# Kernel optimization log

Measured on AMD Instinct MI355X. Metric: run time of the kernel, lower is better.

## Reference

```python
import jax, jax.numpy as jnp
import numpy as np

IN_DIM, H, OUT_DIM = 64, 128, 64
B, T = 1024, 512
NEG_SLOPE = 0.01
LN_EPS = 1e-5


def _mlp_layer(x, W, b, g, beta):
    h = x @ W.T + b
    h = jnp.where(h > 0, h, NEG_SLOPE * h)  # LeakyReLU
    mu = h.mean(-1, keepdims=True)
    var = h.var(-1, keepdims=True)
    return g * (h - mu) / jnp.sqrt(var + LN_EPS) + beta


def setup_inputs() -> dict:
    key = jax.random.key(0)
    ks = jax.random.split(key, 16)
    s = 1.0 / np.sqrt(H)
    return {
        "x": jax.random.normal(ks[0], (B, T, IN_DIM), jnp.float32),
        "is_init": jax.random.randint(ks[1], (B, T, 1), 0, 2) > 0,
        "hx": jax.random.normal(ks[2], (B, H), jnp.float32),
        "W1": jax.random.uniform(ks[3], (H, IN_DIM), jnp.float32, -s, s),
        "b1": jnp.zeros((H,), jnp.float32),
        "g1": jnp.ones((H,), jnp.float32),
        "beta1": jnp.zeros((H,), jnp.float32),
        "W2": jax.random.uniform(ks[4], (H, H), jnp.float32, -s, s),
        "b2": jnp.zeros((H,), jnp.float32),
        "g2": jnp.ones((H,), jnp.float32),
        "beta2": jnp.zeros((H,), jnp.float32),
        "W_ih": jax.random.uniform(ks[5], (3 * H, H), jnp.float32, -s, s),
        "W_hh": jax.random.uniform(ks[6], (3 * H, H), jnp.float32, -s, s),
        "b_ih": jax.random.uniform(ks[7], (3 * H,), jnp.float32, -s, s),
        "b_hh": jax.random.uniform(ks[8], (3 * H,), jnp.float32, -s, s),
        "W_out": jax.random.uniform(ks[9], (OUT_DIM, H), jnp.float32, -s, s),
        "b_out": jnp.zeros((OUT_DIM,), jnp.float32),
    }


def reference(x, is_init, hx, W1, b1, g1, beta1, W2, b2, g2, beta2,
              W_ih, W_hh, b_ih, b_hh, W_out, b_out):
    # MLP: two (Linear -> LeakyReLU -> LayerNorm) layers, width 128
    h = _mlp_layer(x, W1, b1, g1, beta1)
    h = _mlp_layer(h, W2, b2, g2, beta2)

    # Precompute input-side gate preactivations for all timesteps: [B,T,3H]
    gates_x = h @ W_ih.T + b_ih
    gates_x_t = jnp.swapaxes(gates_x, 0, 1)      # [T,B,3H]
    init_t = jnp.swapaxes(is_init, 0, 1)         # [T,B,1]

    def step(h_prev, inp):
        gx, init = inp
        h_prev = jnp.where(init, 0.0, h_prev)    # reset-on-init
        gh = h_prev @ W_hh.T + b_hh
        xr, xz, xn = jnp.split(gx, 3, axis=-1)
        hr, hz, hn = jnp.split(gh, 3, axis=-1)
        r = jax.nn.sigmoid(xr + hr)
        z = jax.nn.sigmoid(xz + hz)
        n = jnp.tanh(xn + r * hn)
        h_new = (1.0 - z) * n + z * h_prev
        return h_new, h_new

    hx_final, ys = jax.lax.scan(step, hx, (gates_x_t, init_t))
    y = jnp.swapaxes(ys, 0, 1)                   # [B,T,H]
    out = y @ W_out.T + b_out                    # [B,T,OUT_DIM]
    return out, hx_final
```

## Files before the change

### kernel.cpp

```cpp
#include <hip/hip_runtime.h>
#include <hip/hip_bf16.h>

#define IN_DIM 64
#define H 128
#define G3 384
#define OUT_DIM 64
#define Bb 1024
#define Tt 512
#define NEG 0.01f
#define EPSLN 1e-5f

#define CHUNK 16
#define NCHUNK (Tt / CHUNK)
#define BPB 2

typedef __bf16 bf16_t;
typedef __bf16 bf16x8 __attribute__((ext_vector_type(8)));
typedef float f32x4 __attribute__((ext_vector_type(4)));

#define GXS 392
#define GX_OFF 0
#define HAS 136
#define HA_OFF 25088
#define HPB_OFF 33792
#define RED_OFF 42496
#define MNR_OFF 43520
#define VEC_OFF 43776
#define INI_OFF 50176
#define SMEM_BYTES 50320

#define V_B1 0
#define V_G1 128
#define V_BE1 256
#define V_B2 384
#define V_G2 512
#define V_BE2 640
#define V_BIH 768
#define V_BHH 1152
#define V_BOUT 1536

#define WS_W1 0
#define WS_W2 8192
#define WS_WIH 24576
#define WS_WHH 73728
#define WS_WOUT 122880
#define WS_ELEMS 131072

#define MFMA(a, b, c) __builtin_amdgcn_mfma_f32_16x16x32_bf16((a), (b), (c), 0, 0, 0)

template <bool WSB>
__device__ __forceinline__ bf16x8 ldfrag(const float* pf, const bf16_t* pb) {
    if constexpr (WSB) {
        return *(const bf16x8*)pb;
    } else {
        bf16x8 f;
#pragma unroll
        for (int j = 0; j < 8; ++j) f[j] = (bf16_t)pf[j];
        return f;
    }
}

__global__ void cvt_weights(const float* __restrict__ W1, const float* __restrict__ W2,
                            const float* __restrict__ Wih, const float* __restrict__ Whh,
                            const float* __restrict__ Wout, bf16_t* __restrict__ ws) {
    int i = blockIdx.x * 256 + threadIdx.x;
    float v;
    if (i < WS_W2) v = W1[i];
    else if (i < WS_WIH) v = W2[i - WS_W2];
    else if (i < WS_WHH) v = Wih[i - WS_WIH];
    else if (i < WS_WOUT) v = Whh[i - WS_WHH];
    else v = Wout[i - WS_WOUT];
    ws[i] = (bf16_t)v;
}

template <bool WSB>
__global__ void __launch_bounds__(256, 2) gru_fused(
    const float* __restrict__ x, const int* __restrict__ is_init,
    const float* __restrict__ hx,
    const float* __restrict__ W1, const float* __restrict__ b1,
    const float* __restrict__ g1, const float* __restrict__ be1,
    const float* __restrict__ W2, const float* __restrict__ b2,
    const float* __restrict__ g2, const float* __restrict__ be2,
    const float* __restrict__ Wih, const float* __restrict__ Whh,
    const float* __restrict__ bih, const float* __restrict__ bhh,
    const float* __restrict__ Wout, const float* __restrict__ bout,
    const bf16_t* __restrict__ wsb,
    float* __restrict__ out)
{
    extern __shared__ char smem[];
    bf16_t* GX  = (bf16_t*)(smem + GX_OFF);
    bf16_t* HA  = (bf16_t*)(smem + HA_OFF);
    bf16_t* HPB = (bf16_t*)(smem + HPB_OFF);
    float*  RED = (float*) (smem + RED_OFF);
    float*  MNR = (float*) (smem + MNR_OFF);
    float*  VEC = (float*) (smem + VEC_OFF);
    int*    INI = (int*)   (smem + INI_OFF);

    const bf16_t* W1B  = wsb + WS_W1;
    const bf16_t* W2B  = wsb + WS_W2;
    const bf16_t* WihB = wsb + WS_WIH;
    const bf16_t* WhhB = wsb + WS_WHH;
    const bf16_t* WoB  = wsb + WS_WOUT;

    const int tid  = threadIdx.x;
    const int w    = tid >> 6;
    const int lane = tid & 63;
    const int ln   = lane & 15;
    const int quad = lane >> 4;
    const int b0   = blockIdx.x * BPB;

    for (int i = tid; i < H; i += 256) {
        VEC[V_B1 + i] = b1[i];  VEC[V_G1 + i] = g1[i];  VEC[V_BE1 + i] = be1[i];
        VEC[V_B2 + i] = b2[i];  VEC[V_G2 + i] = g2[i];  VEC[V_BE2 + i] = be2[i];
    }
    for (int i = tid; i < G3; i += 256) {
        VEC[V_BIH + i] = bih[i];  VEC[V_BHH + i] = bhh[i];
    }
    if (tid < OUT_DIM) VEC[V_BOUT + tid] = bout[tid];
    for (int i = tid; i < 2 * 16 * HAS; i += 256) HPB[i] = (bf16_t)0.f;
    __syncthreads();

    float hp[2] = {0.f, 0.f};
    if (quad < BPB) {
        int b = quad;
        int im = is_init[(size_t)(b0 + b) * Tt];
#pragma unroll
        for (int sub = 0; sub < 2; ++sub) {
            int j = w * 32 + sub * 16 + ln;
            float v = im ? 0.f : hx[(size_t)(b0 + b) * H + j];
            hp[sub] = v;
            HPB[b * 4 * HAS + j] = (bf16_t)v;
        }
    }
    float bh[3][2];
#pragma unroll
    for (int g = 0; g < 3; ++g)
#pragma unroll
        for (int sub = 0; sub < 2; ++sub)
            bh[g][sub] = bhh[g * H + w * 32 + sub * 16 + ln];

    bf16x8 whhf[6][4];
#pragma unroll
    for (int ntl = 0; ntl < 6; ++ntl) {
        int gate = ntl >> 1, sub = ntl & 1;
        int n = gate * H + w * 32 + sub * 16 + ln;
#pragma unroll
        for (int ks = 0; ks < 4; ++ks) {
            size_t off = (size_t)n * H + ks * 32 + quad * 8;
            whhf[ntl][ks] = ldfrag<WSB>(Whh + off, WhhB + off);
        }
    }
    __syncthreads();

    for (int tc = 0; tc < NCHUNK; ++tc) {
        const int t0 = tc * CHUNK;

        f32x4 vs[BPB][2];

        {
            bf16x8 w1f[2][2];
#pragma unroll
            for (int ntl = 0; ntl < 2; ++ntl) {
                int n = w * 32 + ntl * 16 + ln;
#pragma unroll
                for (int ks = 0; ks < 2; ++ks) {
                    size_t off = (size_t)n * IN_DIM + ks * 32 + quad * 8;
                    w1f[ntl][ks] = ldfrag<WSB>(W1 + off, W1B + off);
                }
            }
#pragma unroll
            for (int mt = 0; mt < BPB; ++mt) {
                const float* xr_ = x + ((size_t)(b0 + mt) * Tt + t0 + ln) * IN_DIM;
                bf16x8 a0, a1;
#pragma unroll
                for (int j = 0; j < 8; ++j) {
                    a0[j] = (bf16_t)xr_[quad * 8 + j];
                    a1[j] = (bf16_t)xr_[32 + quad * 8 + j];
                }
#pragma unroll
                for (int ntl = 0; ntl < 2; ++ntl) {
                    f32x4 c = {0.f, 0.f, 0.f, 0.f};
                    c = MFMA(a0, w1f[ntl][0], c);
                    c = MFMA(a1, w1f[ntl][1], c);
                    vs[mt][ntl] = c;
                }
            }
            float bv[2], gv[2], bev[2];
#pragma unroll
            for (int ntl = 0; ntl < 2; ++ntl) {
                int n = w * 32 + ntl * 16 + ln;
                bv[ntl] = VEC[V_B1 + n]; gv[ntl] = VEC[V_G1 + n]; bev[ntl] = VEC[V_BE1 + n];
            }
#pragma unroll
            for (int mt = 0; mt < BPB; ++mt) {
#pragma unroll
                for (int reg = 0; reg < 4; ++reg) {
                    float v0 = vs[mt][0][reg] + bv[0]; v0 = v0 > 0.f ? v0 : NEG * v0;
                    float v1 = vs[mt][1][reg] + bv[1]; v1 = v1 > 0.f ? v1 : NEG * v1;
                    vs[mt][0][reg] = v0; vs[mt][1][reg] = v1;
                    float s = v0 + v1, q = v0 * v0 + v1 * v1;
#pragma unroll
                    for (int d = 1; d < 16; d <<= 1) { s += __shfl_xor(s, d); q += __shfl_xor(q, d); }
                    if (ln == 0) {
                        int rr = mt * 16 + quad * 4 + reg;
                        RED[rr * 8 + w] = s; RED[rr * 8 + 4 + w] = q;
                    }
                }
            }
            __syncthreads();
            if (tid < 32) {
                float s = RED[tid * 8] + RED[tid * 8 + 1] + RED[tid * 8 + 2] + RED[tid * 8 + 3];
                float q = RED[tid * 8 + 4] + RED[tid * 8 + 5] + RED[tid * 8 + 6] + RED[tid * 8 + 7];
                float mean = s * (1.f / H);
                float var = q * (1.f / H) - mean * mean;
                MNR[tid * 2] = mean; MNR[tid * 2 + 1] = rsqrtf(var + EPSLN);
            }
            __syncthreads();
#pragma unroll
            for (int mt = 0; mt < BPB; ++mt) {
#pragma unroll
                for (int reg = 0; reg < 4; ++reg) {
                    int rr = mt * 16 + quad * 4 + reg;
                    float mean = MNR[rr * 2], rstd = MNR[rr * 2 + 1];
#pragma unroll
                    for (int ntl = 0; ntl < 2; ++ntl) {
                        int n = w * 32 + ntl * 16 + ln;
                        HA[rr * HAS + n] = (bf16_t)(gv[ntl] * (vs[mt][ntl][reg] - mean) * rstd + bev[ntl]);
                    }
                }
            }
            __syncthreads();
        }

        {
            bf16x8 w2f[2][4];
#pragma unroll
            for (int ntl = 0; ntl < 2; ++ntl) {
                int n = w * 32 + ntl * 16 + ln;
#pragma unroll
                for (int ks = 0; ks < 4; ++ks) {
                    size_t off = (size_t)n * H + ks * 32 + quad * 8;
                    w2f[ntl][ks] = ldfrag<WSB>(W2 + off, W2B + off);
                }
            }
#pragma unroll
            for (int mt = 0; mt < BPB; ++mt) {
                bf16x8 af[4];
#pragma unroll
                for (int ks = 0; ks < 4; ++ks)
                    af[ks] = *(const bf16x8*)(HA + (mt * 16 + ln) * HAS + ks * 32 + quad * 8);
#pragma unroll
                for (int ntl = 0; ntl < 2; ++ntl) {
                    f32x4 c = {0.f, 0.f, 0.f, 0.f};
#pragma unroll
                    for (int ks = 0; ks < 4; ++ks) c = MFMA(af[ks], w2f[ntl][ks], c);
                    vs[mt][ntl] = c;
                }
            }
            float bv[2], gv[2], bev[2];
#pragma unroll
            for (int ntl = 0; ntl < 2; ++ntl) {
                int n = w * 32 + ntl * 16 + ln;
                bv[ntl] = VEC[V_B2 + n]; gv[ntl] = VEC[V_G2 + n]; bev[ntl] = VEC[V_BE2 + n];
            }
#pragma unroll
            for (int mt = 0; mt < BPB; ++mt) {
#pragma unroll
                for (int reg = 0; reg < 4; ++reg) {
                    float v0 = vs[mt][0][reg] + bv[0]; v0 = v0 > 0.f ? v0 : NEG * v0;
                    float v1 = vs[mt][1][reg] + bv[1]; v1 = v1 > 0.f ? v1 : NEG * v1;
                    vs[mt][0][reg] = v0; vs[mt][1][reg] = v1;
                    float s = v0 + v1, q = v0 * v0 + v1 * v1;
#pragma unroll
                    for (int d = 1; d < 16; d <<= 1) { s += __shfl_xor(s, d); q += __shfl_xor(q, d); }
                    if (ln == 0) {
                        int rr = mt * 16 + quad * 4 + reg;
                        RED[rr * 8 + w] = s; RED[rr * 8 + 4 + w] = q;
                    }
                }
            }
            __syncthreads();
            if (tid < 32) {
                float s = RED[tid * 8] + RED[tid * 8 + 1] + RED[tid * 8 + 2] + RED[tid * 8 + 3];
                float q = RED[tid * 8 + 4] + RED[tid * 8 + 5] + RED[tid * 8 + 6] + RED[tid * 8 + 7];
                float mean = s * (1.f / H);
                float var = q * (1.f / H) - mean * mean;
                MNR[tid * 2] = mean; MNR[tid * 2 + 1] = rsqrtf(var + EPSLN);
            }
            __syncthreads();
#pragma unroll
            for (int mt = 0; mt < BPB; ++mt) {
#pragma unroll
                for (int reg = 0; reg < 4; ++reg) {
                    int rr = mt * 16 + quad * 4 + reg;
                    float mean = MNR[rr * 2], rstd = MNR[rr * 2 + 1];
#pragma unroll
                    for (int ntl = 0; ntl < 2; ++ntl) {
                        int n = w * 32 + ntl * 16 + ln;
                        HA[rr * HAS + n] = (bf16_t)(gv[ntl] * (vs[mt][ntl][reg] - mean) * rstd + bev[ntl]);
                    }
                }
            }
            __syncthreads();
        }

#pragma unroll
        for (int half = 0; half < 2; ++half) {
            bf16x8 wf[3][4];
            float bv[3];
#pragma unroll
            for (int k3 = 0; k3 < 3; ++k3) {
                int n = (w * 6 + half * 3 + k3) * 16 + ln;
                bv[k3] = VEC[V_BIH + n];
#pragma unroll
                for (int ks = 0; ks < 4; ++ks) {
                    size_t off = (size_t)n * H + ks * 32 + quad * 8;
                    wf[k3][ks] = ldfrag<WSB>(Wih + off, WihB + off);
                }
            }
#pragma unroll
            for (int mt = 0; mt < BPB; ++mt) {
                bf16x8 af[4];
#pragma unroll
                for (int ks = 0; ks < 4; ++ks)
                    af[ks] = *(const bf16x8*)(HA + (mt * 16 + ln) * HAS + ks * 32 + quad * 8);
#pragma unroll
                for (int k3 = 0; k3 < 3; ++k3) {
                    int n = (w * 6 + half * 3 + k3) * 16 + ln;
                    f32x4 c = {0.f, 0.f, 0.f, 0.f};
#pragma unroll
                    for (int ks = 0; ks < 4; ++ks) c = MFMA(af[ks], wf[k3][ks], c);
#pragma unroll
                    for (int reg = 0; reg < 4; ++reg)
                        GX[(mt * 16 + quad * 4 + reg) * GXS + n] = (bf16_t)(c[reg] + bv[k3]);
                }
            }
        }
        if (tid < BPB * 17) {
            int b = tid / 17, s = tid % 17;
            int t = t0 + s;
            INI[tid] = (t < Tt) ? is_init[(size_t)(b0 + b) * Tt + t] : 0;
        }

        for (int s = 0; s < CHUNK; ++s) {
            __syncthreads();
            const int t = t0 + s;
            const int rp = t & 1;
            bf16x8 af[4];
#pragma unroll
            for (int ks = 0; ks < 4; ++ks)
                af[ks] = *(const bf16x8*)(HPB + rp * 16 * HAS + ln * HAS + ks * 32 + quad * 8);
            f32x4 gc[6];
#pragma unroll
            for (int ntl = 0; ntl < 6; ++ntl) {
                f32x4 c = {0.f, 0.f, 0.f, 0.f};
#pragma unroll
                for (int ks = 0; ks < 4; ++ks) c = MFMA(af[ks], whhf[ntl][ks], c);
                gc[ntl] = c;
            }
            if (quad < BPB) {
                const int b = quad;
                bf16_t* hw = HPB + (rp ^ 1) * 16 * HAS + b * 4 * HAS;
                const int rbase = (b * 16 + s) * GXS;
#pragma unroll
                for (int sub = 0; sub < 2; ++sub) {
                    int j = w * 32 + sub * 16 + ln;
                    float xr = (float)GX[rbase + j];
                    float xz = (float)GX[rbase + H + j];
                    float xn = (float)GX[rbase + 2 * H + j];
                    float hr = gc[sub][0]     + bh[0][sub];
                    float hz = gc[2 + sub][0] + bh[1][sub];
                    float hn = gc[4 + sub][0] + bh[2][sub];
                    float r = 1.f / (1.f + __expf(-(xr + hr)));
                    float z = 1.f / (1.f + __expf(-(xz + hz)));
                    float a = xn + r * hn;
                    a = fminf(fmaxf(a, -15.f), 15.f);
                    float e = __expf(-2.f * a);
                    float nn = (1.f - e) / (1.f + e);
                    float hnew = (1.f - z) * nn + z * hp[sub];
                    HA[(b * 16 + s) * HAS + j] = (bf16_t)hnew;
                    float hm;
                    if (t < Tt - 1) {
                        hm = INI[b * 17 + s + 1] ? 0.f : hnew;
                    } else {
                        hm = hnew;
                        out[(size_t)Bb * Tt * OUT_DIM + (size_t)(b0 + b) * H + j] = hnew;
                    }
                    hp[sub] = hm;
                    hw[j] = (bf16_t)hm;
                }
            }
        }
        __syncthreads();

        {
            int o = w * 16 + ln;
            size_t ob = (size_t)o * H;
            bf16x8 wof[4];
#pragma unroll
            for (int ks = 0; ks < 4; ++ks)
                wof[ks] = ldfrag<WSB>(Wout + ob + ks * 32 + quad * 8, WoB + ob + ks * 32 + quad * 8);
            float bo = VEC[V_BOUT + o];
#pragma unroll
            for (int mt = 0; mt < BPB; ++mt) {
                bf16x8 af[4];
#pragma unroll
                for (int ks = 0; ks < 4; ++ks)
                    af[ks] = *(const bf16x8*)(HA + (mt * 16 + ln) * HAS + ks * 32 + quad * 8);
                f32x4 c = {0.f, 0.f, 0.f, 0.f};
#pragma unroll
                for (int ks = 0; ks < 4; ++ks) c = MFMA(af[ks], wof[ks], c);
#pragma unroll
                for (int reg = 0; reg < 4; ++reg)
                    out[((size_t)(b0 + mt) * Tt + t0 + quad * 4 + reg) * OUT_DIM + o] = c[reg] + bo;
            }
        }
        __syncthreads();
    }
}

extern "C" void kernel_launch(void* const* d_in, const int* in_sizes, int n_in,
                              void* d_out, int out_size, void* d_ws, size_t ws_size,
                              hipStream_t stream) {
    const float* x      = (const float*)d_in[0];
    const int*   is_init= (const int*)  d_in[1];
    const float* hx     = (const float*)d_in[2];
    const float* W1     = (const float*)d_in[3];
    const float* b1     = (const float*)d_in[4];
    const float* g1     = (const float*)d_in[5];
    const float* be1    = (const float*)d_in[6];
    const float* W2     = (const float*)d_in[7];
    const float* b2     = (const float*)d_in[8];
    const float* g2     = (const float*)d_in[9];
    const float* be2    = (const float*)d_in[10];
    const float* Wih    = (const float*)d_in[11];
    const float* Whh    = (const float*)d_in[12];
    const float* bih    = (const float*)d_in[13];
    const float* bhh    = (const float*)d_in[14];
    const float* Wout   = (const float*)d_in[15];
    const float* bout   = (const float*)d_in[16];
    float* out = (float*)d_out;

    const bool usews = (d_ws != nullptr) && (ws_size >= (size_t)(WS_ELEMS * sizeof(bf16_t)));
    if (usews) {
        bf16_t* ws = (bf16_t*)d_ws;
        cvt_weights<<<WS_ELEMS / 256, 256, 0, stream>>>(W1, W2, Wih, Whh, Wout, ws);
        hipFuncSetAttribute((const void*)gru_fused<true>,
                            hipFuncAttributeMaxDynamicSharedMemorySize, SMEM_BYTES);
        gru_fused<true><<<Bb / BPB, 256, SMEM_BYTES, stream>>>(
            x, is_init, hx, W1, b1, g1, be1, W2, b2, g2, be2,
            Wih, Whh, bih, bhh, Wout, bout, ws, out);
    } else {
        hipFuncSetAttribute((const void*)gru_fused<false>,
                            hipFuncAttributeMaxDynamicSharedMemorySize, SMEM_BYTES);
        gru_fused<false><<<Bb / BPB, 256, SMEM_BYTES, stream>>>(
            x, is_init, hx, W1, b1, g1, be1, W2, b2, g2, be2,
            Wih, Whh, bih, bhh, Wout, bout, nullptr, out);
    }
}
```

Baseline: 1.402 ms.

## Parallelize GRU scan over time tiles with speculative pass and fix-up passes

Replaces the sequential per-batch scan with a time-tiled scheme. All 32 time tiles run in parallel from a zero (or reset) initial state, and each tile records its end state and whether it starts with a reset. A fix-up kernel reruns the prefix of each tile up to the first reset, using the previous tile's end state, and a sweep kernel propagates corrections for tiles whose state depends on earlier tiles. This exposes far more parallelism than one block per two batch rows. In exchange it adds redundant MLP and GRU recomputation, extra workspace traffic and a sequential sweep whose cost depends on how often resets occur.

```diff
diff --git a/kernel.cpp b/kernel.cpp
--- a/kernel.cpp
+++ b/kernel.cpp
@@ -11,33 +11,13 @@
 #define EPSLN 1e-5f
 
 #define CHUNK 16
-#define NCHUNK (Tt / CHUNK)
-#define BPB 2
+#define NTILE (Tt / CHUNK)
 
 typedef __bf16 bf16_t;
 typedef __bf16 bf16x8 __attribute__((ext_vector_type(8)));
 typedef float f32x4 __attribute__((ext_vector_type(4)));
 
-#define GXS 392
-#define GX_OFF 0
-#define HAS 136
-#define HA_OFF 25088
-#define HPB_OFF 33792
-#define RED_OFF 42496
-#define MNR_OFF 43520
-#define VEC_OFF 43776
-#define INI_OFF 50176
-#define SMEM_BYTES 50320
-
-#define V_B1 0
-#define V_G1 128
-#define V_BE1 256
-#define V_B2 384
-#define V_G2 512
-#define V_BE2 640
-#define V_BIH 768
-#define V_BHH 1152
-#define V_BOUT 1536
+#define MFMA(a, b, c) __builtin_amdgcn_mfma_f32_16x16x32_bf16((a), (b), (c), 0, 0, 0)
 
 #define WS_W1 0
 #define WS_W2 8192
@@ -45,24 +25,18 @@
 #define WS_WHH 73728
 #define WS_WOUT 122880
 #define WS_ELEMS 131072
-
-#define MFMA(a, b, c) __builtin_amdgcn_mfma_f32_16x16x32_bf16((a), (b), (c), 0, 0, 0)
-
-template <bool WSB>
-__device__ __forceinline__ bf16x8 ldfrag(const float* pf, const bf16_t* pb) {
-    if constexpr (WSB) {
-        return *(const bf16x8*)pb;
-    } else {
-        bf16x8 f;
-#pragma unroll
-        for (int j = 0; j < 8; ++j) f[j] = (bf16_t)pf[j];
-        return f;
-    }
-}
+#define WS_E_OFF 262144
+#define WS_R_OFF (WS_E_OFF + 16777216)
+#define WS_RA_OFF (WS_R_OFF + 131072)
+#define WS_NEED (WS_RA_OFF + 131072)
+
+#define HAS 136
+#define GXS 392
 
 __global__ void cvt_weights(const float* __restrict__ W1, const float* __restrict__ W2,
                             const float* __restrict__ Wih, const float* __restrict__ Whh,
-                            const float* __restrict__ Wout, bf16_t* __restrict__ ws) {
+                            const float* __restrict__ Wout, bf16_t* __restrict__ ws,
+                            int* __restrict__ RA) {
     int i = blockIdx.x * 256 + threadIdx.x;
     float v;
     if (i < WS_W2) v = W1[i];
@@ -71,10 +45,764 @@
     else if (i < WS_WOUT) v = Whh[i - WS_WHH];
     else v = Wout[i - WS_WOUT];
     ws[i] = (bf16_t)v;
+    if (i < Bb * NTILE) RA[i] = 0;
 }
 
-template <bool WSB>
-__global__ void __launch_bounds__(256, 2) gru_fused(
+#define P1_GX 0
+#define P1_HA 50176
+#define P1_HPB 67584
+#define P1_RED 76288
+#define P1_MNR 78336
+#define P1_INI 78848
+#define P1_SMEM 79120
+#define BPB1 4
+
+__global__ void __launch_bounds__(256, 2) gru_pass1(
+    const float* __restrict__ x, const int* __restrict__ is_init,
+    const float* __restrict__ hx,
+    const float* __restrict__ b1, const float* __restrict__ g1, const float* __restrict__ be1,
+    const float* __restrict__ b2, const float* __restrict__ g2, const float* __restrict__ be2,
+    const float* __restrict__ bih, const float* __restrict__ bhh,
+    const float* __restrict__ bout,
+    const bf16_t* __restrict__ wsb,
+    float* __restrict__ E, int* __restrict__ R,
+    float* __restrict__ out)
+{
+    extern __shared__ char smem[];
+    bf16_t* GX  = (bf16_t*)(smem + P1_GX);
+    bf16_t* HA  = (bf16_t*)(smem + P1_HA);
+    bf16_t* HPB = (bf16_t*)(smem + P1_HPB);
+    float*  RED = (float*) (smem + P1_RED);
+    float*  MNR = (float*) (smem + P1_MNR);
+    int*    INI = (int*)   (smem + P1_INI);
+
+    const bf16_t* W1B  = wsb + WS_W1;
+    const bf16_t* W2B  = wsb + WS_W2;
+    const bf16_t* WihB = wsb + WS_WIH;
+    const bf16_t* WhhB = wsb + WS_WHH;
+    const bf16_t* WoB  = wsb + WS_WOUT;
+
+    const int tid  = threadIdx.x;
+    const int w    = tid >> 6;
+    const int lane = tid & 63;
+    const int ln   = lane & 15;
+    const int quad = lane >> 4;
+    const int b0   = blockIdx.x * BPB1;
+    const int tile = blockIdx.y;
+    const int t0   = tile * CHUNK;
+
+    for (int i = tid; i < 2 * 16 * HAS; i += 256) HPB[i] = (bf16_t)0.f;
+    __syncthreads();
+
+    float hp[2] = {0.f, 0.f};
+    if (tile == 0) {
+        const int b = quad;
+        int im = is_init[(size_t)(b0 + b) * Tt];
+#pragma unroll
+        for (int sub = 0; sub < 2; ++sub) {
+            int j = w * 32 + sub * 16 + ln;
+            float v = im ? 0.f : hx[(size_t)(b0 + b) * H + j];
+            hp[sub] = v;
+            HPB[b * 4 * HAS + j] = (bf16_t)v;
+        }
+    }
+    float bh[3][2];
+#pragma unroll
+    for (int g = 0; g < 3; ++g)
+#pragma unroll
+        for (int sub = 0; sub < 2; ++sub)
+            bh[g][sub] = bhh[g * H + w * 32 + sub * 16 + ln];
+
+    bf16x8 whhf[6][4];
+#pragma unroll
+    for (int ntl = 0; ntl < 6; ++ntl) {
+        int gate = ntl >> 1, sub = ntl & 1;
+        int n = gate * H + w * 32 + sub * 16 + ln;
+#pragma unroll
+        for (int ks = 0; ks < 4; ++ks)
+            whhf[ntl][ks] = *(const bf16x8*)(WhhB + (size_t)n * H + ks * 32 + quad * 8);
+    }
+    __syncthreads();
+
+    f32x4 vs[BPB1][2];
+
+    {
+        bf16x8 w1f[2][2];
+#pragma unroll
+        for (int ntl = 0; ntl < 2; ++ntl) {
+            int n = w * 32 + ntl * 16 + ln;
+#pragma unroll
+            for (int ks = 0; ks < 2; ++ks)
+                w1f[ntl][ks] = *(const bf16x8*)(W1B + (size_t)n * IN_DIM + ks * 32 + quad * 8);
+        }
+#pragma unroll
+        for (int mt = 0; mt < BPB1; ++mt) {
+            const float* xr_ = x + ((size_t)(b0 + mt) * Tt + t0 + ln) * IN_DIM;
+            bf16x8 a0, a1;
+#pragma unroll
+            for (int j = 0; j < 8; ++j) {
+                a0[j] = (bf16_t)xr_[quad * 8 + j];
+                a1[j] = (bf16_t)xr_[32 + quad * 8 + j];
+            }
+#pragma unroll
+            for (int ntl = 0; ntl < 2; ++ntl) {
+                f32x4 c = {0.f, 0.f, 0.f, 0.f};
+                c = MFMA(a0, w1f[ntl][0], c);
+                c = MFMA(a1, w1f[ntl][1], c);
+                vs[mt][ntl] = c;
+            }
+        }
+        float bv[2], gv[2], bev[2];
+#pragma unroll
+        for (int ntl = 0; ntl < 2; ++ntl) {
+            int n = w * 32 + ntl * 16 + ln;
+            bv[ntl] = b1[n]; gv[ntl] = g1[n]; bev[ntl] = be1[n];
+        }
+#pragma unroll
+        for (int mt = 0; mt < BPB1; ++mt) {
+#pragma unroll
+            for (int reg = 0; reg < 4; ++reg) {
+                float v0 = vs[mt][0][reg] + bv[0]; v0 = v0 > 0.f ? v0 : NEG * v0;
+                float v1 = vs[mt][1][reg] + bv[1]; v1 = v1 > 0.f ? v1 : NEG * v1;
+                vs[mt][0][reg] = v0; vs[mt][1][reg] = v1;
+                float s = v0 + v1, q = v0 * v0 + v1 * v1;
+#pragma unroll
+                for (int d = 1; d < 16; d <<= 1) { s += __shfl_xor(s, d); q += __shfl_xor(q, d); }
+                if (ln == 0) {
+                    int rr = mt * 16 + quad * 4 + reg;
+                    RED[rr * 8 + w] = s; RED[rr * 8 + 4 + w] = q;
+                }
+            }
+        }
+        __syncthreads();
+        if (tid < 64) {
+            float s = RED[tid * 8] + RED[tid * 8 + 1] + RED[tid * 8 + 2] + RED[tid * 8 + 3];
+            float q = RED[tid * 8 + 4] + RED[tid * 8 + 5] + RED[tid * 8 + 6] + RED[tid * 8 + 7];
+            float mean = s * (1.f / H);
+            float var = q * (1.f / H) - mean * mean;
+            MNR[tid * 2] = mean; MNR[tid * 2 + 1] = rsqrtf(var + EPSLN);
+        }
+        __syncthreads();
+#pragma unroll
+        for (int mt = 0; mt < BPB1; ++mt) {
+#pragma unroll
+            for (int reg = 0; reg < 4; ++reg) {
+                int rr = mt * 16 + quad * 4 + reg;
+                float mean = MNR[rr * 2], rstd = MNR[rr * 2 + 1];
+#pragma unroll
+                for (int ntl = 0; ntl < 2; ++ntl) {
+                    int n = w * 32 + ntl * 16 + ln;
+                    HA[rr * HAS + n] = (bf16_t)(gv[ntl] * (vs[mt][ntl][reg] - mean) * rstd + bev[ntl]);
+                }
+            }
+        }
+        __syncthreads();
+    }
+
+    {
+        bf16x8 w2f[2][4];
+#pragma unroll
+        for (int ntl = 0; ntl < 2; ++ntl) {
+            int n = w * 32 + ntl * 16 + ln;
+#pragma unroll
+            for (int ks = 0; ks < 4; ++ks)
+                w2f[ntl][ks] = *(const bf16x8*)(W2B + (size_t)n * H + ks * 32 + quad * 8);
+        }
+#pragma unroll
+        for (int mt = 0; mt < BPB1; ++mt) {
+            bf16x8 af[4];
+#pragma unroll
+            for (int ks = 0; ks < 4; ++ks)
+                af[ks] = *(const bf16x8*)(HA + (mt * 16 + ln) * HAS + ks * 32 + quad * 8);
+#pragma unroll
+            for (int ntl = 0; ntl < 2; ++ntl) {
+                f32x4 c = {0.f, 0.f, 0.f, 0.f};
+#pragma unroll
+                for (int ks = 0; ks < 4; ++ks) c = MFMA(af[ks], w2f[ntl][ks], c);
+                vs[mt][ntl] = c;
+            }
+        }
+        float bv[2], gv[2], bev[2];
+#pragma unroll
+        for (int ntl = 0; ntl < 2; ++ntl) {
+            int n = w * 32 + ntl * 16 + ln;
+            bv[ntl] = b2[n]; gv[ntl] = g2[n]; bev[ntl] = be2[n];
+        }
+#pragma unroll
+        for (int mt = 0; mt < BPB1; ++mt) {
+#pragma unroll
+            for (int reg = 0; reg < 4; ++reg) {
+                float v0 = vs[mt][0][reg] + bv[0]; v0 = v0 > 0.f ? v0 : NEG * v0;
+                float v1 = vs[mt][1][reg] + bv[1]; v1 = v1 > 0.f ? v1 : NEG * v1;
+                vs[mt][0][reg] = v0; vs[mt][1][reg] = v1;
+                float s = v0 + v1, q = v0 * v0 + v1 * v1;
+#pragma unroll
+                for (int d = 1; d < 16; d <<= 1) { s += __shfl_xor(s, d); q += __shfl_xor(q, d); }
+                if (ln == 0) {
+                    int rr = mt * 16 + quad * 4 + reg;
+                    RED[rr * 8 + w] = s; RED[rr * 8 + 4 + w] = q;
+                }
+            }
+        }
+        __syncthreads();
+        if (tid < 64) {
+            float s = RED[tid * 8] + RED[tid * 8 + 1] + RED[tid * 8 + 2] + RED[tid * 8 + 3];
+            float q = RED[tid * 8 + 4] + RED[tid * 8 + 5] + RED[tid * 8 + 6] + RED[tid * 8 + 7];
+            float mean = s * (1.f / H);
+            float var = q * (1.f / H) - mean * mean;
+            MNR[tid * 2] = mean; MNR[tid * 2 + 1] = rsqrtf(var + EPSLN);
+        }
+        __syncthreads();
+#pragma unroll
+        for (int mt = 0; mt < BPB1; ++mt) {
+#pragma unroll
+            for (int reg = 0; reg < 4; ++reg) {
+                int rr = mt * 16 + quad * 4 + reg;
+                float mean = MNR[rr * 2], rstd = MNR[rr * 2 + 1];
+#pragma unroll
+                for (int ntl = 0; ntl < 2; ++ntl) {
+                    int n = w * 32 + ntl * 16 + ln;
+                    HA[rr * HAS + n] = (bf16_t)(gv[ntl] * (vs[mt][ntl][reg] - mean) * rstd + bev[ntl]);
+                }
+            }
+        }
+        __syncthreads();
+    }
+
+#pragma unroll
+    for (int half = 0; half < 2; ++half) {
+        bf16x8 wf[3][4];
+        float bv[3];
+#pragma unroll
+        for (int k3 = 0; k3 < 3; ++k3) {
+            int n = (w * 6 + half * 3 + k3) * 16 + ln;
+            bv[k3] = bih[n];
+#pragma unroll
+            for (int ks = 0; ks < 4; ++ks)
+                wf[k3][ks] = *(const bf16x8*)(WihB + (size_t)n * H + ks * 32 + quad * 8);
+        }
+#pragma unroll
+        for (int mt = 0; mt < BPB1; ++mt) {
+            bf16x8 af[4];
+#pragma unroll
+            for (int ks = 0; ks < 4; ++ks)
+                af[ks] = *(const bf16x8*)(HA + (mt * 16 + ln) * HAS + ks * 32 + quad * 8);
+#pragma unroll
+            for (int k3 = 0; k3 < 3; ++k3) {
+                int n = (w * 6 + half * 3 + k3) * 16 + ln;
+                f32x4 c = {0.f, 0.f, 0.f, 0.f};
+#pragma unroll
+                for (int ks = 0; ks < 4; ++ks) c = MFMA(af[ks], wf[k3][ks], c);
+#pragma unroll
+                for (int reg = 0; reg < 4; ++reg)
+                    GX[(mt * 16 + quad * 4 + reg) * GXS + n] = (bf16_t)(c[reg] + bv[k3]);
+            }
+        }
+    }
+    if (tid < BPB1 * 17) {
+        int b = tid / 17, s = tid % 17;
+        int t = t0 + s;
+        INI[tid] = (t < Tt) ? is_init[(size_t)(b0 + b) * Tt + t] : 0;
+    }
+
+    for (int s = 0; s < CHUNK; ++s) {
+        __syncthreads();
+        const int t = t0 + s;
+        const int rp = t & 1;
+        bf16x8 af[4];
+#pragma unroll
+        for (int ks = 0; ks < 4; ++ks)
+            af[ks] = *(const bf16x8*)(HPB + rp * 16 * HAS + ln * HAS + ks * 32 + quad * 8);
+        f32x4 gc[6];
+#pragma unroll
+        for (int ntl = 0; ntl < 6; ++ntl) {
+            f32x4 c = {0.f, 0.f, 0.f, 0.f};
+#pragma unroll
+            for (int ks = 0; ks < 4; ++ks) c = MFMA(af[ks], whhf[ntl][ks], c);
+            gc[ntl] = c;
+        }
+        {
+            const int b = quad;
+            bf16_t* hw = HPB + (rp ^ 1) * 16 * HAS + b * 4 * HAS;
+            const int rbase = (b * 16 + s) * GXS;
+#pragma unroll
+            for (int sub = 0; sub < 2; ++sub) {
+                int j = w * 32 + sub * 16 + ln;
+                float xr = (float)GX[rbase + j];
+                float xz = (float)GX[rbase + H + j];
+                float xn = (float)GX[rbase + 2 * H + j];
+                float hr = gc[sub][0]     + bh[0][sub];
+                float hz = gc[2 + sub][0] + bh[1][sub];
+                float hn = gc[4 + sub][0] + bh[2][sub];
+                float r = 1.f / (1.f + __expf(-(xr + hr)));
+                float z = 1.f / (1.f + __expf(-(xz + hz)));
+                float a = xn + r * hn;
+                a = fminf(fmaxf(a, -15.f), 15.f);
+                float e = __expf(-2.f * a);
+                float nn = (1.f - e) / (1.f + e);
+                float hnew = (1.f - z) * nn + z * hp[sub];
+                HA[(b * 16 + s) * HAS + j] = (bf16_t)hnew;
+                float hm;
+                if (s < CHUNK - 1) {
+                    hm = INI[b * 17 + s + 1] ? 0.f : hnew;
+                } else {
+                    hm = hnew;
+                    E[((size_t)(b0 + b) * NTILE + tile) * H + j] = hnew;
+                }
+                hp[sub] = hm;
+                hw[j] = (bf16_t)hm;
+            }
+        }
+    }
+    __syncthreads();
+
+    if (tid < BPB1) {
+        int any = 0;
+#pragma unroll
+        for (int s = 0; s < CHUNK; ++s) any |= INI[tid * 17 + s];
+        R[(b0 + tid) * NTILE + tile] = (tile == 0) ? 1 : (any ? 1 : 0);
+    }
+
+    {
+        int o = w * 16 + ln;
+        bf16x8 wof[4];
+#pragma unroll
+        for (int ks = 0; ks < 4; ++ks)
+            wof[ks] = *(const bf16x8*)(WoB + (size_t)o * H + ks * 32 + quad * 8);
+        float bo = bout[o];
+#pragma unroll
+        for (int mt = 0; mt < BPB1; ++mt) {
+            bf16x8 af[4];
+#pragma unroll
+            for (int ks = 0; ks < 4; ++ks)
+                af[ks] = *(const bf16x8*)(HA + (mt * 16 + ln) * HAS + ks * 32 + quad * 8);
+            f32x4 c = {0.f, 0.f, 0.f, 0.f};
+#pragma unroll
+            for (int ks = 0; ks < 4; ++ks) c = MFMA(af[ks], wof[ks], c);
+#pragma unroll
+            for (int reg = 0; reg < 4; ++reg)
+                out[((size_t)(b0 + mt) * Tt + t0 + quad * 4 + reg) * OUT_DIM + o] = c[reg] + bo;
+        }
+    }
+}
+
+__global__ void __launch_bounds__(256, 2) gru_fixp(
+    const float* __restrict__ x, const int* __restrict__ is_init,
+    const float* __restrict__ b1, const float* __restrict__ g1, const float* __restrict__ be1,
+    const float* __restrict__ b2, const float* __restrict__ g2, const float* __restrict__ be2,
+    const float* __restrict__ bih, const float* __restrict__ bhh,
+    const float* __restrict__ bout,
+    const bf16_t* __restrict__ wsb,
+    float* __restrict__ E, const int* __restrict__ R, int* __restrict__ RA,
+    float* __restrict__ out)
+{
+    __shared__ bf16_t sHA[16 * HAS];
+    __shared__ bf16_t sHPB[2][16 * HAS];
+    __shared__ float  sHPF[16 * 128];
+    __shared__ float  sRED[16 * 8];
+    __shared__ float  sMNR[16 * 2];
+    __shared__ int    sINI[16 * 16];
+    __shared__ int    sF[16];
+    __shared__ int    sNeed[16];
+    __shared__ int    sAny, sMaxf;
+
+    const bf16_t* W1B  = wsb + WS_W1;
+    const bf16_t* W2B  = wsb + WS_W2;
+    const bf16_t* WihB = wsb + WS_WIH;
+    const bf16_t* WhhB = wsb + WS_WHH;
+    const bf16_t* WoB  = wsb + WS_WOUT;
+
+    const int tid  = threadIdx.x;
+    const int w    = tid >> 6;
+    const int lane = tid & 63;
+    const int ln   = lane & 15;
+    const int quad = lane >> 4;
+    const int bB   = blockIdx.x * 16;
+    const int i    = blockIdx.y + 1;
+    const int t0   = i * CHUNK;
+
+    {
+        int b = tid >> 4, s = tid & 15;
+        sINI[tid] = is_init[(size_t)(bB + b) * Tt + t0 + s];
+    }
+    if (tid < 16) sNeed[tid] = R[(bB + tid) * NTILE + (i - 1)];
+    if (tid == 0) { sAny = 0; sMaxf = 0; }
+    __syncthreads();
+    if (tid < 16) {
+        int f = 16;
+        for (int s = 15; s >= 0; --s) if (sINI[tid * 16 + s]) f = s;
+        sF[tid] = f;
+        int need = (sNeed[tid] && f > 0) ? 1 : 0;
+        sNeed[tid] = need;
+        if (need) { atomicOr(&sAny, 1); atomicMax(&sMaxf, f); }
+    }
+    __syncthreads();
+    if (!sAny) return;
+    const int maxf = sMaxf;
+
+    for (int idx = tid; idx < 16 * 128; idx += 256) {
+        int b = idx >> 7, j = idx & 127;
+        float v = sNeed[b] ? E[((size_t)(bB + b) * NTILE + i - 1) * H + j] : 0.f;
+        sHPF[idx] = v;
+        sHPB[0][b * HAS + j] = (bf16_t)v;
+        sHPB[1][b * HAS + j] = (bf16_t)0.f;
+    }
+
+    float bh[3][2], bihv[6];
+#pragma unroll
+    for (int g = 0; g < 3; ++g)
+#pragma unroll
+        for (int sub = 0; sub < 2; ++sub) {
+            int j = w * 32 + sub * 16 + ln;
+            bh[g][sub] = bhh[g * H + j];
+            bihv[g * 2 + sub] = bih[g * H + j];
+        }
+    float bv1[2], gv1[2], bev1[2], bv2[2], gv2[2], bev2[2];
+#pragma unroll
+    for (int ntl = 0; ntl < 2; ++ntl) {
+        int n = w * 32 + ntl * 16 + ln;
+        bv1[ntl] = b1[n]; gv1[ntl] = g1[n]; bev1[ntl] = be1[n];
+        bv2[ntl] = b2[n]; gv2[ntl] = g2[n]; bev2[ntl] = be2[n];
+    }
+    bf16x8 whhf[6][4];
+#pragma unroll
+    for (int ntl = 0; ntl < 6; ++ntl) {
+        int gate = ntl >> 1, sub = ntl & 1;
+        int n = gate * H + w * 32 + sub * 16 + ln;
+#pragma unroll
+        for (int ks = 0; ks < 4; ++ks)
+            whhf[ntl][ks] = *(const bf16x8*)(WhhB + (size_t)n * H + ks * 32 + quad * 8);
+    }
+    bf16x8 wof[4];
+    {
+        int o = w * 16 + ln;
+#pragma unroll
+        for (int ks = 0; ks < 4; ++ks)
+            wof[ks] = *(const bf16x8*)(WoB + (size_t)o * H + ks * 32 + quad * 8);
+    }
+    float bo = bout[w * 16 + ln];
+    __syncthreads();
+
+    for (int s = 0; s < maxf; ++s) {
+        const int t = t0 + s;
+        const int par = s & 1;
+        f32x4 vs[2];
+
+        {
+            const float* xr_ = x + ((size_t)(bB + ln) * Tt + t) * IN_DIM;
+            bf16x8 a0, a1;
+#pragma unroll
+            for (int j = 0; j < 8; ++j) {
+                a0[j] = (bf16_t)xr_[quad * 8 + j];
+                a1[j] = (bf16_t)xr_[32 + quad * 8 + j];
+            }
+#pragma unroll
+            for (int ntl = 0; ntl < 2; ++ntl) {
+                int n = w * 32 + ntl * 16 + ln;
+                bf16x8 f0 = *(const bf16x8*)(W1B + (size_t)n * IN_DIM + quad * 8);
+                bf16x8 f1 = *(const bf16x8*)(W1B + (size_t)n * IN_DIM + 32 + quad * 8);
+                f32x4 c = {0.f, 0.f, 0.f, 0.f};
+                c = MFMA(a0, f0, c);
+                c = MFMA(a1, f1, c);
+                vs[ntl] = c;
+            }
+        }
+#pragma unroll
+        for (int reg = 0; reg < 4; ++reg) {
+            float v0 = vs[0][reg] + bv1[0]; v0 = v0 > 0.f ? v0 : NEG * v0;
+            float v1 = vs[1][reg] + bv1[1]; v1 = v1 > 0.f ? v1 : NEG * v1;
+            vs[0][reg] = v0; vs[1][reg] = v1;
+            float sm = v0 + v1, q = v0 * v0 + v1 * v1;
+#pragma unroll
+            for (int d = 1; d < 16; d <<= 1) { sm += __shfl_xor(sm, d); q += __shfl_xor(q, d); }
+            if (ln == 0) {
+                int rr = quad * 4 + reg;
+                sRED[rr * 8 + w] = sm; sRED[rr * 8 + 4 + w] = q;
+            }
+        }
+        __syncthreads();
+        if (tid < 16) {
+            float sm = sRED[tid * 8] + sRED[tid * 8 + 1] + sRED[tid * 8 + 2] + sRED[tid * 8 + 3];
+            float q = sRED[tid * 8 + 4] + sRED[tid * 8 + 5] + sRED[tid * 8 + 6] + sRED[tid * 8 + 7];
+            float mean = sm * (1.f / H);
+            float var = q * (1.f / H) - mean * mean;
+            sMNR[tid * 2] = mean; sMNR[tid * 2 + 1] = rsqrtf(var + EPSLN);
+        }
+        __syncthreads();
+#pragma unroll
+        for (int reg = 0; reg < 4; ++reg) {
+            int rr = quad * 4 + reg;
+            float mean = sMNR[rr * 2], rstd = sMNR[rr * 2 + 1];
+#pragma unroll
+            for (int ntl = 0; ntl < 2; ++ntl) {
+                int n = w * 32 + ntl * 16 + ln;
+                sHA[rr * HAS + n] = (bf16_t)(gv1[ntl] * (vs[ntl][reg] - mean) * rstd + bev1[ntl]);
+            }
+        }
+        __syncthreads();
+
+        {
+            bf16x8 af[4];
+#pragma unroll
+            for (int ks = 0; ks < 4; ++ks)
+                af[ks] = *(const bf16x8*)(sHA + ln * HAS + ks * 32 + quad * 8);
+#pragma unroll
+            for (int ntl = 0; ntl < 2; ++ntl) {
+                int n = w * 32 + ntl * 16 + ln;
+                f32x4 c = {0.f, 0.f, 0.f, 0.f};
+#pragma unroll
+                for (int ks = 0; ks < 4; ++ks) {
+                    bf16x8 f = *(const bf16x8*)(W2B + (size_t)n * H + ks * 32 + quad * 8);
+                    c = MFMA(af[ks], f, c);
+                }
+                vs[ntl] = c;
+            }
+        }
+        __syncthreads();
+#pragma unroll
+        for (int reg = 0; reg < 4; ++reg) {
+            float v0 = vs[0][reg] + bv2[0]; v0 = v0 > 0.f ? v0 : NEG * v0;
+            float v1 = vs[1][reg] + bv2[1]; v1 = v1 > 0.f ? v1 : NEG * v1;
+            vs[0][reg] = v0; vs[1][reg] = v1;
+            float sm = v0 + v1, q = v0 * v0 + v1 * v1;
+#pragma unroll
+            for (int d = 1; d < 16; d <<= 1) { sm += __shfl_xor(sm, d); q += __shfl_xor(q, d); }
+            if (ln == 0) {
+                int rr = quad * 4 + reg;
+                sRED[rr * 8 + w] = sm; sRED[rr * 8 + 4 + w] = q;
+            }
+        }
+        __syncthreads();
+        if (tid < 16) {
+            float sm = sRED[tid * 8] + sRED[tid * 8 + 1] + sRED[tid * 8 + 2] + sRED[tid * 8 + 3];
+            float q = sRED[tid * 8 + 4] + sRED[tid * 8 + 5] + sRED[tid * 8 + 6] + sRED[tid * 8 + 7];
+            float mean = sm * (1.f / H);
+            float var = q * (1.f / H) - mean * mean;
+            sMNR[tid * 2] = mean; sMNR[tid * 2 + 1] = rsqrtf(var + EPSLN);
+        }
+        __syncthreads();
+#pragma unroll
+        for (int reg = 0; reg < 4; ++reg) {
+            int rr = quad * 4 + reg;
+            float mean = sMNR[rr * 2], rstd = sMNR[rr * 2 + 1];
+#pragma unroll
+            for (int ntl = 0; ntl < 2; ++ntl) {
+                int n = w * 32 + ntl * 16 + ln;
+                sHA[rr * HAS + n] = (bf16_t)(gv2[ntl] * (vs[ntl][reg] - mean) * rstd + bev2[ntl]);
+            }
+        }
+        __syncthreads();
+
+        bf16x8 af2[4], afh[4];
+#pragma unroll
+        for (int ks = 0; ks < 4; ++ks) {
+            af2[ks] = *(const bf16x8*)(sHA + ln * HAS + ks * 32 + quad * 8);
+            afh[ks] = *(const bf16x8*)(sHPB[par] + ln * HAS + ks * 32 + quad * 8);
+        }
+        f32x4 gxc[6], ghc[6];
+#pragma unroll
+        for (int ntl = 0; ntl < 6; ++ntl) {
+            int gate = ntl >> 1, sub = ntl & 1;
+            int n = gate * H + w * 32 + sub * 16 + ln;
+            f32x4 cg = {0.f, 0.f, 0.f, 0.f};
+#pragma unroll
+            for (int ks = 0; ks < 4; ++ks) {
+                bf16x8 f = *(const bf16x8*)(WihB + (size_t)n * H + ks * 32 + quad * 8);
+                cg = MFMA(af2[ks], f, cg);
+            }
+            gxc[ntl] = cg;
+            f32x4 ch = {0.f, 0.f, 0.f, 0.f};
+#pragma unroll
+            for (int ks = 0; ks < 4; ++ks) ch = MFMA(afh[ks], whhf[ntl][ks], ch);
+            ghc[ntl] = ch;
+        }
+        __syncthreads();
+
+#pragma unroll
+        for (int reg = 0; reg < 4; ++reg) {
+            const int b = quad * 4 + reg;
+            const int msk = sNeed[b] && (s < sF[b]);
+#pragma unroll
+            for (int sub = 0; sub < 2; ++sub) {
+                int j = w * 32 + sub * 16 + ln;
+                float xr = gxc[sub][reg]     + bihv[sub];
+                float xz = gxc[2 + sub][reg] + bihv[2 + sub];
+                float xn = gxc[4 + sub][reg] + bihv[4 + sub];
+                float hr = ghc[sub][reg]     + bh[0][sub];
+                float hz = ghc[2 + sub][reg] + bh[1][sub];
+                float hn = ghc[4 + sub][reg] + bh[2][sub];
+                float r = 1.f / (1.f + __expf(-(xr + hr)));
+                float z = 1.f / (1.f + __expf(-(xz + hz)));
+                float a = xn + r * hn;
+                a = fminf(fmaxf(a, -15.f), 15.f);
+                float e = __expf(-2.f * a);
+                float nn = (1.f - e) / (1.f + e);
+                float hp = sHPF[b * 128 + j];
+                float hnew = (1.f - z) * nn + z * hp;
+                if (msk) {
+                    sHPF[b * 128 + j] = hnew;
+                    sHPB[par ^ 1][b * HAS + j] = (bf16_t)hnew;
+                    sHA[b * HAS + j] = (bf16_t)hnew;
+                }
+            }
+        }
+        __syncthreads();
+
+        {
+            bf16x8 af[4];
+#pragma unroll
+            for (int ks = 0; ks < 4; ++ks)
+                af[ks] = *(const bf16x8*)(sHA + ln * HAS + ks * 32 + quad * 8);
+            f32x4 c = {0.f, 0.f, 0.f, 0.f};
+#pragma unroll
+            for (int ks = 0; ks < 4; ++ks) c = MFMA(af[ks], wof[ks], c);
+            int o = w * 16 + ln;
+#pragma unroll
+            for (int reg = 0; reg < 4; ++reg) {
+                int b = quad * 4 + reg;
+                if (sNeed[b] && s < sF[b])
+                    out[((size_t)(bB + b) * Tt + t) * OUT_DIM + o] = c[reg] + bo;
+            }
+        }
+        __syncthreads();
+    }
+
+    for (int idx = tid; idx < 16 * 128; idx += 256) {
+        int b = idx >> 7, j = idx & 127;
+        if (sNeed[b] && sF[b] == 16)
+            E[((size_t)(bB + b) * NTILE + i) * H + j] = sHPF[b * 128 + j];
+    }
+    if (tid < 16 && sNeed[tid] && sF[tid] == 16)
+        RA[(bB + tid) * NTILE + i] = 1;
+}
+
+__global__ void __launch_bounds__(128) gru_sweep(
+    const float* __restrict__ x, const int* __restrict__ is_init,
+    const float* __restrict__ W1, const float* __restrict__ b1,
+    const float* __restrict__ g1, const float* __restrict__ be1,
+    const float* __restrict__ W2, const float* __restrict__ b2,
+    const float* __restrict__ g2, const float* __restrict__ be2,
+    const float* __restrict__ Wih, const float* __restrict__ Whh,
+    const float* __restrict__ bih, const float* __restrict__ bhh,
+    const float* __restrict__ Wout, const float* __restrict__ bout,
+    const float* __restrict__ E, const int* __restrict__ R, const int* __restrict__ RA,
+    float* __restrict__ out)
+{
+    __shared__ float sX[64], sH1[128], sH2[128], sHH[128], sRS[4];
+    __shared__ int sI[16], sFf;
+
+    const int b = blockIdx.x;
+    const int j = threadIdx.x;
+    const int wv = j >> 6, lj = j & 63;
+
+    float h = E[((size_t)b * NTILE) * H + j];
+
+    for (int i = 1; i < NTILE; ++i) {
+        int Rm1 = R[b * NTILE + i - 1];
+        if (!Rm1) {
+            if (j < 16) sI[j] = is_init[(size_t)b * Tt + i * CHUNK + j];
+            __syncthreads();
+            if (j == 0) {
+                int f = 16;
+                for (int s = 15; s >= 0; --s) if (sI[s]) f = s;
+                sFf = f;
+            }
+            __syncthreads();
+            int f = sFf;
+            for (int s = 0; s < f; ++s) {
+                int t = i * CHUNK + s;
+                sHH[j] = h;
+                if (j < 64) sX[j] = x[((size_t)b * Tt + t) * IN_DIM + j];
+                __syncthreads();
+                float a1 = b1[j];
+                const float* w1r = W1 + (size_t)j * IN_DIM;
+                for (int k = 0; k < 64; ++k) a1 += sX[k] * w1r[k];
+                a1 = a1 > 0.f ? a1 : NEG * a1;
+                {
+                    float sv = a1, sq = a1 * a1;
+                    for (int d = 1; d < 64; d <<= 1) { sv += __shfl_xor(sv, d); sq += __shfl_xor(sq, d); }
+                    if (lj == 0) { sRS[wv * 2] = sv; sRS[wv * 2 + 1] = sq; }
+                    __syncthreads();
+                    float mean = (sRS[0] + sRS[2]) * (1.f / H);
+                    float var = (sRS[1] + sRS[3]) * (1.f / H) - mean * mean;
+                    a1 = g1[j] * (a1 - mean) * rsqrtf(var + EPSLN) + be1[j];
+                }
+                sH1[j] = a1;
+                __syncthreads();
+                float a2 = b2[j];
+                const float* w2r = W2 + (size_t)j * H;
+                for (int k = 0; k < 128; ++k) a2 += sH1[k] * w2r[k];
+                a2 = a2 > 0.f ? a2 : NEG * a2;
+                {
+                    float sv = a2, sq = a2 * a2;
+                    for (int d = 1; d < 64; d <<= 1) { sv += __shfl_xor(sv, d); sq += __shfl_xor(sq, d); }
+                    if (lj == 0) { sRS[wv * 2] = sv; sRS[wv * 2 + 1] = sq; }
+                    __syncthreads();
+                    float mean = (sRS[0] + sRS[2]) * (1.f / H);
+                    float var = (sRS[1] + sRS[3]) * (1.f / H) - mean * mean;
+                    a2 = g2[j] * (a2 - mean) * rsqrtf(var + EPSLN) + be2[j];
+                }
+                sH2[j] = a2;
+                __syncthreads();
+                float gx0 = bih[j], gx1 = bih[H + j], gx2 = bih[2 * H + j];
+                float gh0 = bhh[j], gh1 = bhh[H + j], gh2 = bhh[2 * H + j];
+                const float* wi0 = Wih + (size_t)j * H;
+                const float* wi1 = Wih + (size_t)(H + j) * H;
+                const float* wi2 = Wih + (size_t)(2 * H + j) * H;
+                const float* wh0 = Whh + (size_t)j * H;
+                const float* wh1 = Whh + (size_t)(H + j) * H;
+                const float* wh2 = Whh + (size_t)(2 * H + j) * H;
+                for (int k = 0; k < 128; ++k) {
+                    float h2k = sH2[k], hhk = sHH[k];
+                    gx0 += h2k * wi0[k]; gx1 += h2k * wi1[k]; gx2 += h2k * wi2[k];
+                    gh0 += hhk * wh0[k]; gh1 += hhk * wh1[k]; gh2 += hhk * wh2[k];
+                }
+                float r = 1.f / (1.f + __expf(-(gx0 + gh0)));
+                float z = 1.f / (1.f + __expf(-(gx1 + gh1)));
+                float a = gx2 + r * gh2;
+                a = fminf(fmaxf(a, -15.f), 15.f);
+                float e = __expf(-2.f * a);
+                float nn = (1.f - e) / (1.f + e);
+                h = (1.f - z) * nn + z * h;
+                __syncthreads();
+                sH1[j] = h;
+                __syncthreads();
+                if (j < 64) {
+                    float o = bout[j];
+                    const float* wo = Wout + (size_t)j * H;
+                    for (int k = 0; k < 128; ++k) o += sH1[k] * wo[k];
+                    out[((size_t)b * Tt + t) * OUT_DIM + j] = o;
+                }
+                __syncthreads();
+            }
+            if (f < 16) h = E[((size_t)b * NTILE + i) * H + j];
+        } else {
+            if (R[b * NTILE + i] || RA[b * NTILE + i])
+                h = E[((size_t)b * NTILE + i) * H + j];
+        }
+    }
+    out[(size_t)Bb * Tt * OUT_DIM + (size_t)b * H + j] = h;
+}
+
+#define FGX_OFF 0
+#define FHA_OFF 25088
+#define FHPB_OFF 33792
+#define FRED_OFF 42496
+#define FMNR_OFF 43520
+#define FVEC_OFF 43776
+#define FINI_OFF 50176
+#define FSMEM 50320
+#define FV_B1 0
+#define FV_G1 128
+#define FV_BE1 256
+#define FV_B2 384
+#define FV_G2 512
+#define FV_BE2 640
+#define FV_BIH 768
+#define FV_BHH 1152
+#define FV_BOUT 1536
+
+__global__ void __launch_bounds__(256, 2) gru_seq(
     const float* __restrict__ x, const int* __restrict__ is_init,
     const float* __restrict__ hx,
     const float* __restrict__ W1, const float* __restrict__ b1,
@@ -84,52 +812,45 @@
     const float* __restrict__ Wih, const float* __restrict__ Whh,
     const float* __restrict__ bih, const float* __restrict__ bhh,
     const float* __restrict__ Wout, const float* __restrict__ bout,
-    const bf16_t* __restrict__ wsb,
     float* __restrict__ out)
 {
     extern __shared__ char smem[];
-    bf16_t* GX  = (bf16_t*)(smem + GX_OFF);
-    bf16_t* HA  = (bf16_t*)(smem + HA_OFF);
-    bf16_t* HPB = (bf16_t*)(smem + HPB_OFF);
-    float*  RED = (float*) (smem + RED_OFF);
-    float*  MNR = (float*) (smem + MNR_OFF);
-    float*  VEC = (float*) (smem + VEC_OFF);
-    int*    INI = (int*)   (smem + INI_OFF);
-
-    const bf16_t* W1B  = wsb + WS_W1;
-    const bf16_t* W2B  = wsb + WS_W2;
-    const bf16_t* WihB = wsb + WS_WIH;
-    const bf16_t* WhhB = wsb + WS_WHH;
-    const bf16_t* WoB  = wsb + WS_WOUT;
+    bf16_t* GX  = (bf16_t*)(smem + FGX_OFF);
+    bf16_t* HA  = (bf16_t*)(smem + FHA_OFF);
+    bf16_t* HPB = (bf16_t*)(smem + FHPB_OFF);
+    float*  RED = (float*) (smem + FRED_OFF);
+    float*  MNR = (float*) (smem + FMNR_OFF);
+    float*  VEC = (float*) (smem + FVEC_OFF);
+    int*    INI = (int*)   (smem + FINI_OFF);
 
     const int tid  = threadIdx.x;
     const int w    = tid >> 6;
     const int lane = tid & 63;
     const int ln   = lane & 15;
     const int quad = lane >> 4;
-    const int b0   = blockIdx.x * BPB;
+    const int b0   = blockIdx.x * 2;
 
     for (int i = tid; i < H; i += 256) {
-        VEC[V_B1 + i] = b1[i];  VEC[V_G1 + i] = g1[i];  VEC[V_BE1 + i] = be1[i];
-        VEC[V_B2 + i] = b2[i];  VEC[V_G2 + i] = g2[i];  VEC[V_BE2 + i] = be2[i];
+        VEC[FV_B1 + i] = b1[i];  VEC[FV_G1 + i] = g1[i];  VEC[FV_BE1 + i] = be1[i];
+        VEC[FV_B2 + i] = b2[i];  VEC[FV_G2 + i] = g2[i];  VEC[FV_BE2 + i] = be2[i];
     }
     for (int i = tid; i < G3; i += 256) {
-        VEC[V_BIH + i] = bih[i];  VEC[V_BHH + i] = bhh[i];
-    }
-    if (tid < OUT_DIM) VEC[V_BOUT + tid] = bout[tid];
+        VEC[FV_BIH + i] = bih[i];  VEC[FV_BHH + i] = bhh[i];
+    }
+    if (tid < OUT_DIM) VEC[FV_BOUT + tid] = bout[tid];
     for (int i = tid; i < 2 * 16 * HAS; i += 256) HPB[i] = (bf16_t)0.f;
     __syncthreads();
 
     float hp[2] = {0.f, 0.f};
-    if (quad < BPB) {
+    if (quad < 2) {
         int b = quad;
         int im = is_init[(size_t)(b0 + b) * Tt];
 #pragma unroll
         for (int sub = 0; sub < 2; ++sub) {
-            int j = w * 32 + sub * 16 + ln;
-            float v = im ? 0.f : hx[(size_t)(b0 + b) * H + j];
+            int jj = w * 32 + sub * 16 + ln;
+            float v = im ? 0.f : hx[(size_t)(b0 + b) * H + jj];
             hp[sub] = v;
-            HPB[b * 4 * HAS + j] = (bf16_t)v;
+            HPB[b * 4 * HAS + jj] = (bf16_t)v;
         }
     }
     float bh[3][2];
@@ -144,38 +865,44 @@
     for (int ntl = 0; ntl < 6; ++ntl) {
         int gate = ntl >> 1, sub = ntl & 1;
         int n = gate * H + w * 32 + sub * 16 + ln;
+        const float* p = Whh + (size_t)n * H;
 #pragma unroll
         for (int ks = 0; ks < 4; ++ks) {
-            size_t off = (size_t)n * H + ks * 32 + quad * 8;
-            whhf[ntl][ks] = ldfrag<WSB>(Whh + off, WhhB + off);
+            const float* q = p + ks * 32 + quad * 8;
+            bf16x8 f;
+#pragma unroll
+            for (int jj = 0; jj < 8; ++jj) f[jj] = (bf16_t)q[jj];
+            whhf[ntl][ks] = f;
         }
     }
     __syncthreads();
 
-    for (int tc = 0; tc < NCHUNK; ++tc) {
+    for (int tc = 0; tc < NTILE; ++tc) {
         const int t0 = tc * CHUNK;
-
-        f32x4 vs[BPB][2];
-
+        f32x4 vs[2][2];
         {
             bf16x8 w1f[2][2];
 #pragma unroll
             for (int ntl = 0; ntl < 2; ++ntl) {
                 int n = w * 32 + ntl * 16 + ln;
+                const float* p = W1 + (size_t)n * IN_DIM;
 #pragma unroll
                 for (int ks = 0; ks < 2; ++ks) {
-                    size_t off = (size_t)n * IN_DIM + ks * 32 + quad * 8;
-                    w1f[ntl][ks] = ldfrag<WSB>(W1 + off, W1B + off);
-                }
-            }
-#pragma unroll
-            for (int mt = 0; mt < BPB; ++mt) {
+                    const float* q = p + ks * 32 + quad * 8;
+                    bf16x8 f;
+#pragma unroll
+                    for (int jj = 0; jj < 8; ++jj) f[jj] = (bf16_t)q[jj];
+                    w1f[ntl][ks] = f;
+                }
+            }
+#pragma unroll
+            for (int mt = 0; mt < 2; ++mt) {
                 const float* xr_ = x + ((size_t)(b0 + mt) * Tt + t0 + ln) * IN_DIM;
                 bf16x8 a0, a1;
 #pragma unroll
-                for (int j = 0; j < 8; ++j) {
-                    a0[j] = (bf16_t)xr_[quad * 8 + j];
-                    a1[j] = (bf16_t)xr_[32 + quad * 8 + j];
+                for (int jj = 0; jj < 8; ++jj) {
+                    a0[jj] = (bf16_t)xr_[quad * 8 + jj];
+                    a1[jj] = (bf16_t)xr_[32 + quad * 8 + jj];
                 }
 #pragma unroll
                 for (int ntl = 0; ntl < 2; ++ntl) {
@@ -189,10 +916,10 @@
 #pragma unroll
             for (int ntl = 0; ntl < 2; ++ntl) {
                 int n = w * 32 + ntl * 16 + ln;
-                bv[ntl] = VEC[V_B1 + n]; gv[ntl] = VEC[V_G1 + n]; bev[ntl] = VEC[V_BE1 + n];
-            }
-#pragma unroll
-            for (int mt = 0; mt < BPB; ++mt) {
+                bv[ntl] = VEC[FV_B1 + n]; gv[ntl] = VEC[FV_G1 + n]; bev[ntl] = VEC[FV_BE1 + n];
+            }
+#pragma unroll
+            for (int mt = 0; mt < 2; ++mt) {
 #pragma unroll
                 for (int reg = 0; reg < 4; ++reg) {
                     float v0 = vs[mt][0][reg] + bv[0]; v0 = v0 > 0.f ? v0 : NEG * v0;
@@ -217,7 +944,7 @@
             }
             __syncthreads();
 #pragma unroll
-            for (int mt = 0; mt < BPB; ++mt) {
+            for (int mt = 0; mt < 2; ++mt) {
 #pragma unroll
                 for (int reg = 0; reg < 4; ++reg) {
                     int rr = mt * 16 + quad * 4 + reg;
@@ -231,20 +958,23 @@
             }
             __syncthreads();
         }
-
         {
             bf16x8 w2f[2][4];
 #pragma unroll
             for (int ntl = 0; ntl < 2; ++ntl) {
                 int n = w * 32 + ntl * 16 + ln;
+                const float* p = W2 + (size_t)n * H;
 #pragma unroll
                 for (int ks = 0; ks < 4; ++ks) {
-                    size_t off = (size_t)n * H + ks * 32 + quad * 8;
-                    w2f[ntl][ks] = ldfrag<WSB>(W2 + off, W2B + off);
-                }
-            }
-#pragma unroll
-            for (int mt = 0; mt < BPB; ++mt) {
+                    const float* q = p + ks * 32 + quad * 8;
+                    bf16x8 f;
+#pragma unroll
+                    for (int jj = 0; jj < 8; ++jj) f[jj] = (bf16_t)q[jj];
+                    w2f[ntl][ks] = f;
+                }
+            }
+#pragma unroll
+            for (int mt = 0; mt < 2; ++mt) {
                 bf16x8 af[4];
 #pragma unroll
                 for (int ks = 0; ks < 4; ++ks)
@@ -261,10 +991,10 @@
 #pragma unroll
             for (int ntl = 0; ntl < 2; ++ntl) {
                 int n = w * 32 + ntl * 16 + ln;
-                bv[ntl] = VEC[V_B2 + n]; gv[ntl] = VEC[V_G2 + n]; bev[ntl] = VEC[V_BE2 + n];
-            }
-#pragma unroll
-            for (int mt = 0; mt < BPB; ++mt) {
+                bv[ntl] = VEC[FV_B2 + n]; gv[ntl] = VEC[FV_G2 + n]; bev[ntl] = VEC[FV_BE2 + n];
+            }
+#pragma unroll
+            for (int mt = 0; mt < 2; ++mt) {
 #pragma unroll
                 for (int reg = 0; reg < 4; ++reg) {
                     float v0 = vs[mt][0][reg] + bv[0]; v0 = v0 > 0.f ? v0 : NEG * v0;
@@ -289,7 +1019,7 @@
             }
             __syncthreads();
 #pragma unroll
-            for (int mt = 0; mt < BPB; ++mt) {
+            for (int mt = 0; mt < 2; ++mt) {
 #pragma unroll
                 for (int reg = 0; reg < 4; ++reg) {
                     int rr = mt * 16 + quad * 4 + reg;
@@ -303,7 +1033,6 @@
             }
             __syncthreads();
         }
-
 #pragma unroll
         for (int half = 0; half < 2; ++half) {
             bf16x8 wf[3][4];
@@ -311,15 +1040,19 @@
 #pragma unroll
             for (int k3 = 0; k3 < 3; ++k3) {
                 int n = (w * 6 + half * 3 + k3) * 16 + ln;
-                bv[k3] = VEC[V_BIH + n];
+                bv[k3] = VEC[FV_BIH + n];
+                const float* p = Wih + (size_t)n * H;
 #pragma unroll
                 for (int ks = 0; ks < 4; ++ks) {
-                    size_t off = (size_t)n * H + ks * 32 + quad * 8;
-                    wf[k3][ks] = ldfrag<WSB>(Wih + off, WihB + off);
-                }
-            }
-#pragma unroll
-            for (int mt = 0; mt < BPB; ++mt) {
+                    const float* q = p + ks * 32 + quad * 8;
+                    bf16x8 f;
+#pragma unroll
+                    for (int jj = 0; jj < 8; ++jj) f[jj] = (bf16_t)q[jj];
+                    wf[k3][ks] = f;
+                }
+            }
+#pragma unroll
+            for (int mt = 0; mt < 2; ++mt) {
                 bf16x8 af[4];
 #pragma unroll
                 for (int ks = 0; ks < 4; ++ks)
@@ -336,12 +1069,11 @@
                 }
             }
         }
-        if (tid < BPB * 17) {
+        if (tid < 2 * 17) {
             int b = tid / 17, s = tid % 17;
             int t = t0 + s;
             INI[tid] = (t < Tt) ? is_init[(size_t)(b0 + b) * Tt + t] : 0;
         }
-
         for (int s = 0; s < CHUNK; ++s) {
             __syncthreads();
             const int t = t0 + s;
@@ -358,16 +1090,16 @@
                 for (int ks = 0; ks < 4; ++ks) c = MFMA(af[ks], whhf[ntl][ks], c);
                 gc[ntl] = c;
             }
-            if (quad < BPB) {
+            if (quad < 2) {
                 const int b = quad;
                 bf16_t* hw = HPB + (rp ^ 1) * 16 * HAS + b * 4 * HAS;
                 const int rbase = (b * 16 + s) * GXS;
 #pragma unroll
                 for (int sub = 0; sub < 2; ++sub) {
-                    int j = w * 32 + sub * 16 + ln;
-                    float xr = (float)GX[rbase + j];
-                    float xz = (float)GX[rbase + H + j];
-                    float xn = (float)GX[rbase + 2 * H + j];
+                    int jj = w * 32 + sub * 16 + ln;
+                    float xr = (float)GX[rbase + jj];
+                    float xz = (float)GX[rbase + H + jj];
+                    float xn = (float)GX[rbase + 2 * H + jj];
                     float hr = gc[sub][0]     + bh[0][sub];
                     float hz = gc[2 + sub][0] + bh[1][sub];
                     float hn = gc[4 + sub][0] + bh[2][sub];
@@ -378,31 +1110,35 @@
                     float e = __expf(-2.f * a);
                     float nn = (1.f - e) / (1.f + e);
                     float hnew = (1.f - z) * nn + z * hp[sub];
-                    HA[(b * 16 + s) * HAS + j] = (bf16_t)hnew;
+                    HA[(b * 16 + s) * HAS + jj] = (bf16_t)hnew;
                     float hm;
                     if (t < Tt - 1) {
                         hm = INI[b * 17 + s + 1] ? 0.f : hnew;
                     } else {
                         hm = hnew;
-                        out[(size_t)Bb * Tt * OUT_DIM + (size_t)(b0 + b) * H + j] = hnew;
+                        out[(size_t)Bb * Tt * OUT_DIM + (size_t)(b0 + b) * H + jj] = hnew;
                     }
                     hp[sub] = hm;
-                    hw[j] = (bf16_t)hm;
-                }
-            }
-        }
-        __syncthreads();
-
+                    hw[jj] = (bf16_t)hm;
+                }
+            }
+        }
+        __syncthreads();
         {
             int o = w * 16 + ln;
-            size_t ob = (size_t)o * H;
+            const float* p = Wout + (size_t)o * H;
             bf16x8 wof[4];
 #pragma unroll
-            for (int ks = 0; ks < 4; ++ks)
-                wof[ks] = ldfrag<WSB>(Wout + ob + ks * 32 + quad * 8, WoB + ob + ks * 32 + quad * 8);
-            float bo = VEC[V_BOUT + o];
-#pragma unroll
-            for (int mt = 0; mt < BPB; ++mt) {
+            for (int ks = 0; ks < 4; ++ks) {
+                const float* q = p + ks * 32 + quad * 8;
+                bf16x8 f;
+#pragma unroll
+                for (int jj = 0; jj < 8; ++jj) f[jj] = (bf16_t)q[jj];
+                wof[ks] = f;
+            }
+            float bo = VEC[FV_BOUT + o];
+#pragma unroll
+            for (int mt = 0; mt < 2; ++mt) {
                 bf16x8 af[4];
 #pragma unroll
                 for (int ks = 0; ks < 4; ++ks)
@@ -441,20 +1177,32 @@
     const float* bout   = (const float*)d_in[16];
     float* out = (float*)d_out;
 
-    const bool usews = (d_ws != nullptr) && (ws_size >= (size_t)(WS_ELEMS * sizeof(bf16_t)));
-    if (usews) {
-        bf16_t* ws = (bf16_t*)d_ws;
-        cvt_weights<<<WS_ELEMS / 256, 256, 0, stream>>>(W1, W2, Wih, Whh, Wout, ws);
-        hipFuncSetAttribute((const void*)gru_fused<true>,
-                            hipFuncAttributeMaxDynamicSharedMemorySize, SMEM_BYTES);
-        gru_fused<true><<<Bb / BPB, 256, SMEM_BYTES, stream>>>(
+    if (d_ws != nullptr && ws_size >= (size_t)WS_NEED) {
+        bf16_t* wsb = (bf16_t*)d_ws;
+        float*  E   = (float*)((char*)d_ws + WS_E_OFF);
+        int*    R   = (int*)  ((char*)d_ws + WS_R_OFF);
+        int*    RA  = (int*)  ((char*)d_ws + WS_RA_OFF);
+
+        cvt_weights<<<WS_ELEMS / 256, 256, 0, stream>>>(W1, W2, Wih, Whh, Wout, wsb, RA);
+
+        hipFuncSetAttribute((const void*)gru_pass1,
+                            hipFuncAttributeMaxDynamicSharedMemorySize, P1_SMEM);
+        gru_pass1<<<dim3(Bb / BPB1, NTILE), 256, P1_SMEM, stream>>>(
+            x, is_init, hx, b1, g1, be1, b2, g2, be2, bih, bhh, bout,
+            wsb, E, R, out);
+
+        gru_fixp<<<dim3(Bb / 16, NTILE - 1), 256, 0, stream>>>(
+            x, is_init, b1, g1, be1, b2, g2, be2, bih, bhh, bout,
+            wsb, E, R, RA, out);
+
+        gru_sweep<<<Bb, 128, 0, stream>>>(
+            x, is_init, W1, b1, g1, be1, W2, b2, g2, be2,
+            Wih, Whh, bih, bhh, Wout, bout, E, R, RA, out);
+    } else {
+        hipFuncSetAttribute((const void*)gru_seq,
+                            hipFuncAttributeMaxDynamicSharedMemorySize, FSMEM);
+        gru_seq<<<Bb / 2, 256, FSMEM, stream>>>(
             x, is_init, hx, W1, b1, g1, be1, W2, b2, g2, be2,
-            Wih, Whh, bih, bhh, Wout, bout, ws, out);
-    } else {
-        hipFuncSetAttribute((const void*)gru_fused<false>,
-                            hipFuncAttributeMaxDynamicSharedMemorySize, SMEM_BYTES);
-        gru_fused<false><<<Bb / BPB, 256, SMEM_BYTES, stream>>>(
-            x, is_init, hx, W1, b1, g1, be1, W2, b2, g2, be2,
-            Wih, Whh, bih, bhh, Wout, bout, nullptr, out);
+            Wih, Whh, bih, bhh, Wout, bout, out);
     }
 }
```

Result: faster. 1.346 ms (-4.0%).
